# Kernel tuning notes

Hardware: AMD Instinct MI355X
Metric: run time of the kernel (lower is better)

The kernel has to match this reference:

```python
import jax, jax.numpy as jnp
import numpy as np

EPS_NORM = 1e-12   # F.normalize eps
EPS_PERP = 1e-10   # perplexity log eps
COMMIT = 0.25


def _l2norm(x):
    # matches F.normalize(p=2, dim=1) with eps clamp
    n = jnp.sqrt(jnp.sum(x * x, axis=1, keepdims=True))
    return x / jnp.maximum(n, EPS_NORM)


def setup_inputs() -> dict:
    key = jax.random.key(0)
    k1, k2 = jax.random.split(key)
    B, D, L, K = 8, 256, 4096, 4096
    inputs = jax.random.normal(k1, (B, D, L), dtype=jnp.float32)
    # nn.Embedding init uniform(-1/K, 1/K); use uniform at that scale
    weight = jax.random.uniform(k2, (K, D), minval=-1.0 / K, maxval=1.0 / K, dtype=jnp.float32)
    return {"inputs": inputs, "weight": weight}


def reference(inputs, weight):
    K, D = weight.shape
    x = jnp.transpose(inputs, (0, 2, 1))          # [B, L, D]
    flat = x.reshape(-1, D)                       # [N, D]
    N = flat.shape[0]
    sim = _l2norm(flat) @ _l2norm(weight).T       # [N, K] cosine similarity
    # argmin(1 - sim) == argmax(sim)
    idx = jnp.argmax(sim, axis=1)                 # [N]
    # one-hot @ weight is just a gather of the selected code rows
    quantized = weight[idx].reshape(x.shape)      # [B, L, D]
    e_latent = jnp.mean((jax.lax.stop_gradient(quantized) - x) ** 2)
    q_latent = jnp.mean((quantized - jax.lax.stop_gradient(x)) ** 2)
    loss = q_latent + COMMIT * e_latent
    # straight-through estimator
    q_st = x + jax.lax.stop_gradient(quantized - x)
    # avg_probs = mean of one-hot encodings = normalized histogram of idx
    counts = jnp.zeros((K,), dtype=jnp.float32).at[idx].add(1.0)
    avg_probs = counts / N
    perplexity = jnp.exp(-jnp.sum(avg_probs * jnp.log(avg_probs + EPS_PERP)))
    return jnp.transpose(q_st, (0, 2, 1)), loss, perplexity
```

## Files before the change

### kernel.cpp

```cpp
#include <hip/hip_runtime.h>
#include <stdint.h>

#define Bb 8
#define Dd 256
#define Ll 4096
#define Kk 4096
#define Nn (Bb * Ll)
#define OUT0 (Bb * Dd * Ll)

typedef int    int4v   __attribute__((ext_vector_type(4)));
typedef int    int8v   __attribute__((ext_vector_type(8)));
typedef float  floatx4 __attribute__((ext_vector_type(4)));

#define SCALE1 0x7F7F7F7F

union V8 { int8v v; int4v h[2]; };

__device__ __forceinline__ void async_load16(const void* g, void* l) {
    __builtin_amdgcn_global_load_lds((const __attribute__((address_space(1))) void*)g,
                                     (__attribute__((address_space(3))) void*)l, 16, 0, 0);
}

__global__ void k_prep(const float* __restrict__ w, unsigned char* __restrict__ wn,
                       int* __restrict__ counts) {
    int blk = blockIdx.x, tid = threadIdx.x;
    if (blk == 0)
        for (int i = tid; i < Kk + 2; i += 256) counts[i] = 0;
    int row  = blk * 4 + (tid >> 6);
    int lane = tid & 63;
    float4 v = ((const float4*)(w + (size_t)row * Dd))[lane];
    float ss = v.x*v.x + v.y*v.y + v.z*v.z + v.w*v.w;
#pragma unroll
    for (int m = 1; m < 64; m <<= 1) ss += __shfl_xor(ss, m, 64);
    float s = 16.0f / fmaxf(sqrtf(ss), 1e-12f);
    int p = __builtin_amdgcn_cvt_pk_fp8_f32(v.x * s, v.y * s, 0, false);
    p     = __builtin_amdgcn_cvt_pk_fp8_f32(v.z * s, v.w * s, p, true);
    ((int*)(wn + (size_t)row * Dd))[lane] = p;
}

__global__ __launch_bounds__(512, 2) void k_gemm_fused(
        const float* __restrict__ x, const unsigned char* __restrict__ Wn,
        const float* __restrict__ w, float* __restrict__ out,
        int* __restrict__ counts) {
    union Smem {
        struct { unsigned char As[128 * 256]; unsigned char Bs[2][128 * 256]; } g;
        float wt[64 * 260];
    };
    __shared__ __align__(16) Smem sm;
    __shared__ unsigned int red[128][4];
    __shared__ int kidx[128];
    __shared__ float wsum[8];
    __shared__ int lastsh;

    float* lossacc = (float*)(counts + Kk);
    int*   done    = counts + Kk + 1;

    int bm = blockIdx.x;
    int tid = threadIdx.x, lane = tid & 63, wv = tid >> 6;
    int wm = wv >> 2, wn = wv & 3;
    int l15 = lane & 15, l4 = lane >> 4;

    int goff[4], loff[4];
#pragma unroll
    for (int j = 0; j < 4; ++j) {
        int q = j * 512 + tid;
        int col = q >> 4, p = q & 15;
        goff[j] = col * 256 + ((p ^ (col & 15)) << 4);
        loff[j] = q * 16;
    }

#pragma unroll
    for (int j = 0; j < 4; ++j)
        async_load16(Wn + goff[j], (unsigned char*)sm.g.Bs[0] + loff[j]);

    int b = bm >> 5, l0 = (bm & 31) * 128;
    const float* xs = x + (size_t)b * Dd * Ll + l0;
    int lg = tid & 31, dgr = tid >> 5;
#pragma unroll
    for (int i = 0; i < 4; ++i) {
        int d0 = dgr * 4 + i * 64;
        const float* s0 = xs + (size_t)d0 * Ll + lg * 4;
        float4 f0 = *(const float4*)(s0);
        float4 f1 = *(const float4*)(s0 + Ll);
        float4 f2 = *(const float4*)(s0 + 2 * (size_t)Ll);
        float4 f3 = *(const float4*)(s0 + 3 * (size_t)Ll);
#pragma unroll
        for (int jl = 0; jl < 4; ++jl) {
            float a0 = ((const float*)&f0)[jl], a1 = ((const float*)&f1)[jl];
            float a2 = ((const float*)&f2)[jl], a3 = ((const float*)&f3)[jl];
            int pk = __builtin_amdgcn_cvt_pk_fp8_f32(a0, a1, 0, false);
            pk     = __builtin_amdgcn_cvt_pk_fp8_f32(a2, a3, pk, true);
            int l = lg * 4 + jl;
            *(int*)(sm.g.As + l * 256 + (((d0 >> 4) ^ (l & 15)) << 4) + (d0 & 15)) = pk;
        }
    }
    __syncthreads();

    int8v af[4][2];
#pragma unroll
    for (int fm = 0; fm < 4; ++fm)
#pragma unroll
        for (int ks = 0; ks < 2; ++ks) {
            int l = wm * 64 + fm * 16 + l15;
            int ch = ks * 8 + l4 * 2;
            V8 u;
            u.h[0] = *(const int4v*)(sm.g.As + l * 256 + ((ch ^ l15) << 4));
            u.h[1] = *(const int4v*)(sm.g.As + l * 256 + (((ch + 1) ^ l15) << 4));
            af[fm][ks] = u.v;
        }

    unsigned int rk[4][4];
#pragma unroll
    for (int fm = 0; fm < 4; ++fm)
#pragma unroll
        for (int r = 0; r < 4; ++r) rk[fm][r] = 0u;

    for (int cb = 0; cb < 32; ++cb) {
        int cur = cb & 1;
        if (cb < 31) {
            const unsigned char* g = Wn + (size_t)(cb + 1) * 128 * 256;
            unsigned char* lb = (unsigned char*)sm.g.Bs[cur ^ 1];
#pragma unroll
            for (int j = 0; j < 4; ++j)
                async_load16(g + goff[j], lb + loff[j]);
        }
        const unsigned char* bb = (const unsigned char*)sm.g.Bs[cur];
        int8v bf[2][2];
#pragma unroll
        for (int fn = 0; fn < 2; ++fn)
#pragma unroll
            for (int ks = 0; ks < 2; ++ks) {
                int col = wn * 32 + fn * 16 + l15;
                int ch = ks * 8 + l4 * 2;
                V8 u;
                u.h[0] = *(const int4v*)(bb + col * 256 + ((ch ^ l15) << 4));
                u.h[1] = *(const int4v*)(bb + col * 256 + (((ch + 1) ^ l15) << 4));
                bf[fn][ks] = u.v;
            }
        floatx4 acc[4][2];
#pragma unroll
        for (int fm = 0; fm < 4; ++fm)
#pragma unroll
            for (int fn = 0; fn < 2; ++fn) {
                floatx4 a = (floatx4)512.0f;
                a = __builtin_amdgcn_mfma_scale_f32_16x16x128_f8f6f4(
                        af[fm][0], bf[fn][0], a, 0, 0, 0, SCALE1, 0, SCALE1);
                a = __builtin_amdgcn_mfma_scale_f32_16x16x128_f8f6f4(
                        af[fm][1], bf[fn][1], a, 0, 0, 0, SCALE1, 0, SCALE1);
                acc[fm][fn] = a;
            }
        unsigned int i0 = (unsigned)(cb * 128 + wn * 32 + l15);
#pragma unroll
        for (int fm = 0; fm < 4; ++fm)
#pragma unroll
            for (int r = 0; r < 4; ++r) {
                unsigned int k0 = (__float_as_uint(acc[fm][0][r]) & 0xFFFFF000u) | i0;
                unsigned int k1 = (__float_as_uint(acc[fm][1][r]) & 0xFFFFF000u) | (i0 + 16u);
                unsigned int km = k0 > k1 ? k0 : k1;
                rk[fm][r] = rk[fm][r] > km ? rk[fm][r] : km;
            }
        __syncthreads();
    }

#pragma unroll
    for (int fm = 0; fm < 4; ++fm)
#pragma unroll
        for (int r = 0; r < 4; ++r) {
            unsigned int kx = rk[fm][r];
#pragma unroll
            for (int md = 1; md <= 8; md <<= 1) {
                unsigned int o = (unsigned int)__shfl_xor((int)kx, md, 64);
                kx = kx > o ? kx : o;
            }
            if (l15 == 0) red[wm * 64 + fm * 16 + l4 * 4 + r][wn] = kx;
        }
    __syncthreads();
    if (tid < 128) {
        unsigned int k0 = red[tid][0], k1 = red[tid][1];
        unsigned int k2 = red[tid][2], k3 = red[tid][3];
        unsigned int kx = k0 > k1 ? k0 : k1;
        kx = kx > k2 ? kx : k2;
        kx = kx > k3 ? kx : k3;
        int ix = (int)(kx & 0xFFFu);
        kidx[tid] = ix;
        atomicAdd(&counts[ix], 1);
    }
    __syncthreads();

    float ls = 0.f;
    int fl = tid & 15, dg = tid >> 4;
    size_t xbase = (size_t)b * Dd * Ll + l0 + fl * 4;
    for (int h = 0; h < 2; ++h) {
        float4 xv[8];
        size_t hb = xbase + h * 64;
#pragma unroll
        for (int p = 0; p < 8; ++p)
            xv[p] = *(const float4*)(x + hb + (size_t)(p * 32 + dg) * Ll);

        int rr = tid >> 3, c8 = tid & 7;
        const float* src = w + (size_t)kidx[h * 64 + rr] * Dd + c8 * 4;
        float4 vv[8];
#pragma unroll
        for (int j = 0; j < 8; ++j) vv[j] = *(const float4*)(src + j * 32);
#pragma unroll
        for (int j = 0; j < 8; ++j)
            *(float4*)&sm.wt[rr * 260 + (c8 + j * 8) * 4] = vv[j];
        __syncthreads();

#pragma unroll
        for (int p = 0; p < 8; ++p) {
            int d = p * 32 + dg;
            float4 qv = { sm.wt[(fl * 4 + 0) * 260 + d], sm.wt[(fl * 4 + 1) * 260 + d],
                          sm.wt[(fl * 4 + 2) * 260 + d], sm.wt[(fl * 4 + 3) * 260 + d] };
            float d0 = qv.x - xv[p].x, d1 = qv.y - xv[p].y;
            float d2 = qv.z - xv[p].z, d3 = qv.w - xv[p].w;
            ls += d0 * d0 + d1 * d1 + d2 * d2 + d3 * d3;
            *(float4*)(out + hb + (size_t)d * Ll) = qv;
        }
        __syncthreads();
    }

#pragma unroll
    for (int m = 1; m < 64; m <<= 1) ls += __shfl_xor(ls, m, 64);
    if (lane == 0) wsum[wv] = ls;
    __syncthreads();
    if (tid == 0) {
        atomicAdd(lossacc, wsum[0] + wsum[1] + wsum[2] + wsum[3]
                         + wsum[4] + wsum[5] + wsum[6] + wsum[7]);
        __threadfence();
        lastsh = (atomicAdd(done, 1) == 255);
    }
    __syncthreads();
    if (lastsh) {
        __threadfence();
        float s = 0.f;
        for (int i = tid; i < Kk; i += 512) {
            float p = (float)counts[i] * (1.0f / Nn);
            s += p * logf(p + 1e-10f);
        }
#pragma unroll
        for (int m = 1; m < 64; m <<= 1) s += __shfl_xor(s, m, 64);
        if (lane == 0) wsum[wv] = s;
        __syncthreads();
        if (tid == 0) {
            out[OUT0]     = lossacc[0] * 1.25f / (float)OUT0;
            out[OUT0 + 1] = expf(-(wsum[0] + wsum[1] + wsum[2] + wsum[3]
                                 + wsum[4] + wsum[5] + wsum[6] + wsum[7]));
        }
    }
}

extern "C" void kernel_launch(void* const* d_in, const int* in_sizes, int n_in,
                              void* d_out, int out_size, void* d_ws, size_t ws_size,
                              hipStream_t stream) {
    const float* x = (const float*)d_in[0];
    const float* w = (const float*)d_in[1];
    float* out = (float*)d_out;
    char* ws = (char*)d_ws;

    unsigned char* wn     = (unsigned char*)ws;
    int*           counts = (int*)(ws + (1u << 20));

    k_prep      <<<1024, 256, 0, stream>>>(w, wn, counts);
    k_gemm_fused<<<256,  512, 0, stream>>>(x, wn, w, out, counts);
}
```

Before: 150.1 us.

## Triple-buffer codebook tiles with one barrier per step and register-transpose gather

Replaces the double-buffered codebook tile pipeline with a three-stage ring. Each step waits on vmcnt and issues a single barrier, dropping the trailing __syncthreads, and raises wave priority around the MFMA block. The epilogue no longer stages gathered codebook rows through LDS: each thread loads 4 rows × 4 float4 and transposes them in registers, using the same x access pattern as the prologue. LDS use grows to about 128KB, which may limit occupancy to one block per CU, and the hand-written vmcnt counts depend on how the compiler orders memory operations.

```diff
diff --git a/kernel.cpp b/kernel.cpp
--- a/kernel.cpp
+++ b/kernel.cpp
@@ -42,11 +42,8 @@
         const float* __restrict__ x, const unsigned char* __restrict__ Wn,
         const float* __restrict__ w, float* __restrict__ out,
         int* __restrict__ counts) {
-    union Smem {
-        struct { unsigned char As[128 * 256]; unsigned char Bs[2][128 * 256]; } g;
-        float wt[64 * 260];
-    };
-    __shared__ __align__(16) Smem sm;
+    __shared__ __align__(16) unsigned char As[128 * 256];
+    __shared__ __align__(16) unsigned char Bs[3][128 * 256];
     __shared__ unsigned int red[128][4];
     __shared__ int kidx[128];
     __shared__ float wsum[8];
@@ -71,7 +68,10 @@
 
 #pragma unroll
     for (int j = 0; j < 4; ++j)
-        async_load16(Wn + goff[j], (unsigned char*)sm.g.Bs[0] + loff[j]);
+        async_load16(Wn + goff[j], (unsigned char*)Bs[0] + loff[j]);
+#pragma unroll
+    for (int j = 0; j < 4; ++j)
+        async_load16(Wn + 128 * 256 + goff[j], (unsigned char*)Bs[1] + loff[j]);
 
     int b = bm >> 5, l0 = (bm & 31) * 128;
     const float* xs = x + (size_t)b * Dd * Ll + l0;
@@ -91,7 +91,7 @@
             int pk = __builtin_amdgcn_cvt_pk_fp8_f32(a0, a1, 0, false);
             pk     = __builtin_amdgcn_cvt_pk_fp8_f32(a2, a3, pk, true);
             int l = lg * 4 + jl;
-            *(int*)(sm.g.As + l * 256 + (((d0 >> 4) ^ (l & 15)) << 4) + (d0 & 15)) = pk;
+            *(int*)(As + l * 256 + (((d0 >> 4) ^ (l & 15)) << 4) + (d0 & 15)) = pk;
         }
     }
     __syncthreads();
@@ -104,8 +104,8 @@
             int l = wm * 64 + fm * 16 + l15;
             int ch = ks * 8 + l4 * 2;
             V8 u;
-            u.h[0] = *(const int4v*)(sm.g.As + l * 256 + ((ch ^ l15) << 4));
-            u.h[1] = *(const int4v*)(sm.g.As + l * 256 + (((ch + 1) ^ l15) << 4));
+            u.h[0] = *(const int4v*)(As + l * 256 + ((ch ^ l15) << 4));
+            u.h[1] = *(const int4v*)(As + l * 256 + (((ch + 1) ^ l15) << 4));
             af[fm][ks] = u.v;
         }
 
@@ -116,15 +116,18 @@
         for (int r = 0; r < 4; ++r) rk[fm][r] = 0u;
 
     for (int cb = 0; cb < 32; ++cb) {
-        int cur = cb & 1;
-        if (cb < 31) {
-            const unsigned char* g = Wn + (size_t)(cb + 1) * 128 * 256;
-            unsigned char* lb = (unsigned char*)sm.g.Bs[cur ^ 1];
+        if (cb == 31) asm volatile("s_waitcnt vmcnt(0)" ::: "memory");
+        else          asm volatile("s_waitcnt vmcnt(4)" ::: "memory");
+        __builtin_amdgcn_s_barrier();
+        __builtin_amdgcn_sched_barrier(0);
+        if (cb <= 29) {
+            const unsigned char* g = Wn + (size_t)(cb + 2) * (128 * 256);
+            unsigned char* lb = (unsigned char*)Bs[(cb + 2) % 3];
 #pragma unroll
             for (int j = 0; j < 4; ++j)
                 async_load16(g + goff[j], lb + loff[j]);
         }
-        const unsigned char* bb = (const unsigned char*)sm.g.Bs[cur];
+        const unsigned char* bb = (const unsigned char*)Bs[cb % 3];
         int8v bf[2][2];
 #pragma unroll
         for (int fn = 0; fn < 2; ++fn)
@@ -137,6 +140,7 @@
                 u.h[1] = *(const int4v*)(bb + col * 256 + (((ch + 1) ^ l15) << 4));
                 bf[fn][ks] = u.v;
             }
+        __builtin_amdgcn_s_setprio(1);
         floatx4 acc[4][2];
 #pragma unroll
         for (int fm = 0; fm < 4; ++fm)
@@ -149,6 +153,7 @@
                         af[fm][1], bf[fn][1], a, 0, 0, 0, SCALE1, 0, SCALE1);
                 acc[fm][fn] = a;
             }
+        __builtin_amdgcn_s_setprio(0);
         unsigned int i0 = (unsigned)(cb * 128 + wn * 32 + l15);
 #pragma unroll
         for (int fm = 0; fm < 4; ++fm)
@@ -159,7 +164,6 @@
                 unsigned int km = k0 > k1 ? k0 : k1;
                 rk[fm][r] = rk[fm][r] > km ? rk[fm][r] : km;
             }
-        __syncthreads();
     }
 
 #pragma unroll
@@ -188,36 +192,41 @@
     __syncthreads();
 
     float ls = 0.f;
-    int fl = tid & 15, dg = tid >> 4;
-    size_t xbase = (size_t)b * Dd * Ll + l0 + fl * 4;
-    for (int h = 0; h < 2; ++h) {
-        float4 xv[8];
-        size_t hb = xbase + h * 64;
-#pragma unroll
-        for (int p = 0; p < 8; ++p)
-            xv[p] = *(const float4*)(x + hb + (size_t)(p * 32 + dg) * Ll);
-
-        int rr = tid >> 3, c8 = tid & 7;
-        const float* src = w + (size_t)kidx[h * 64 + rr] * Dd + c8 * 4;
-        float4 vv[8];
-#pragma unroll
-        for (int j = 0; j < 8; ++j) vv[j] = *(const float4*)(src + j * 32);
-#pragma unroll
-        for (int j = 0; j < 8; ++j)
-            *(float4*)&sm.wt[rr * 260 + (c8 + j * 8) * 4] = vv[j];
-        __syncthreads();
-
-#pragma unroll
-        for (int p = 0; p < 8; ++p) {
-            int d = p * 32 + dg;
-            float4 qv = { sm.wt[(fl * 4 + 0) * 260 + d], sm.wt[(fl * 4 + 1) * 260 + d],
-                          sm.wt[(fl * 4 + 2) * 260 + d], sm.wt[(fl * 4 + 3) * 260 + d] };
-            float d0 = qv.x - xv[p].x, d1 = qv.y - xv[p].y;
-            float d2 = qv.z - xv[p].z, d3 = qv.w - xv[p].w;
-            ls += d0 * d0 + d1 * d1 + d2 * d2 + d3 * d3;
-            *(float4*)(out + hb + (size_t)d * Ll) = qv;
-        }
-        __syncthreads();
+    {
+        float4 xv4[4][4];
+#pragma unroll
+        for (int i = 0; i < 4; ++i) {
+            const float* s0 = xs + (size_t)(dgr * 4 + i * 64) * Ll + lg * 4;
+            xv4[i][0] = *(const float4*)(s0);
+            xv4[i][1] = *(const float4*)(s0 + Ll);
+            xv4[i][2] = *(const float4*)(s0 + 2 * (size_t)Ll);
+            xv4[i][3] = *(const float4*)(s0 + 3 * (size_t)Ll);
+        }
+        float4 q4[4][4];
+        int r0 = lg * 4;
+#pragma unroll
+        for (int jl = 0; jl < 4; ++jl) {
+            const float* wr = w + (size_t)kidx[r0 + jl] * Dd + dgr * 4;
+#pragma unroll
+            for (int i = 0; i < 4; ++i)
+                q4[jl][i] = *(const float4*)(wr + i * 64);
+        }
+        float* os = out + (size_t)b * Dd * Ll + l0 + lg * 4;
+#pragma unroll
+        for (int i = 0; i < 4; ++i)
+#pragma unroll
+            for (int dd = 0; dd < 4; ++dd) {
+                float4 qq;
+                qq.x = ((const float*)&q4[0][i])[dd];
+                qq.y = ((const float*)&q4[1][i])[dd];
+                qq.z = ((const float*)&q4[2][i])[dd];
+                qq.w = ((const float*)&q4[3][i])[dd];
+                float4 xv = xv4[i][dd];
+                float e0 = qq.x - xv.x, e1 = qq.y - xv.y;
+                float e2 = qq.z - xv.z, e3 = qq.w - xv.w;
+                ls += e0*e0 + e1*e1 + e2*e2 + e3*e3;
+                *(float4*)(os + (size_t)(dgr * 4 + i * 64 + dd) * Ll) = qq;
+            }
     }
 
 #pragma unroll
```

Result: no change. 150.2 us (+0.1%).
